# Optimization experiments

Measured on AMD Instinct MI355X. Metric: run time of the kernel, lower is better.

Reference implementation:

```python
import jax, jax.numpy as jnp
import numpy as np

N_NODES = 50000
N_EDGES = 1_600_000
IN_FEAT = 128
OUT_FEAT = 128
NUM_RELS = 8


def setup_inputs() -> dict:
    key = jax.random.key(0)
    k_h, k_src, k_dst, k_et, k_nrm, k_w, k_b = jax.random.split(key, 7)
    h = jax.random.normal(k_h, (N_NODES, IN_FEAT), dtype=jnp.float32)
    src = jax.random.randint(k_src, (N_EDGES,), 0, N_NODES, dtype=jnp.int32)
    dst = jax.random.randint(k_dst, (N_EDGES,), 0, N_NODES, dtype=jnp.int32)
    etype = jax.random.randint(k_et, (N_EDGES,), 0, NUM_RELS, dtype=jnp.int32)
    norm = jax.random.uniform(k_nrm, (N_EDGES, 1), dtype=jnp.float32)
    W = jax.random.normal(k_w, (NUM_RELS, IN_FEAT, OUT_FEAT), dtype=jnp.float32)
    b = jax.random.normal(k_b, (NUM_RELS, OUT_FEAT), dtype=jnp.float32)
    return {"h": h, "src": src, "dst": dst, "etype": etype, "norm": norm, "W": W, "b": b}


def reference(h, src, dst, etype, norm, W, b):
    # Per-relation node transforms: [R, N, out]. Same math as the DGL code
    # (which computes src_h @ W for all relations then gathers the right one
    # per edge), but computed once per node instead of once per edge.
    H = jnp.einsum('ni,rio->rno', h, W)
    # Gather per-edge transformed message, add per-relation bias, scale by norm.
    msg = (H[etype, src] + b[etype]) * norm  # [E, out]
    # Sum-reduce messages into destination nodes.
    out = jax.ops.segment_sum(msg, dst, num_segments=h.shape[0])  # [N, out]
    return jax.nn.relu(out)
```

## Files before the change

### kernel.cpp

```cpp
#include <hip/hip_runtime.h>

#define N_NODES_C   50000
#define N_EDGES_C   1600000
#define FEAT        128
#define NREL        8
#define NBUCKETS    400000
#define KTOT        1024
#define TILE        16

#define WS3_COUNTS   0
#define WS3_OFFSETS  400000
#define WS3_RANK     2000000
#define WS3_BSUM     3600000
#define WS3_BOFF     3602048
#define WS3_SORTED   3604096
#define WS3_HB       10004096
#define WS3_WT       22804096
#define WS3_NEEDED   23066240

typedef __attribute__((ext_vector_type(8))) short bf16x8;
typedef __attribute__((ext_vector_type(4))) float f32x4;

__device__ __forceinline__ unsigned short f2bf(float f) {
    unsigned u = __float_as_uint(f);
    return (unsigned short)((u + 0x7fffu + ((u >> 16) & 1u)) >> 16);
}
__device__ __forceinline__ float bf2f(unsigned short b) {
    return __uint_as_float((unsigned)b << 16);
}
__device__ __forceinline__ float lo16(unsigned u) { return __uint_as_float(u << 16); }
__device__ __forceinline__ float hi16(unsigned u) { return __uint_as_float(u & 0xffff0000u); }

__global__ void k_prep(const float* __restrict__ h, const float* __restrict__ W,
                       unsigned* __restrict__ counts, unsigned short* __restrict__ hb,
                       unsigned short* __restrict__ wt) {
    int b = blockIdx.x, t = threadIdx.x;
    if (b < 3125) {
        int i = (b * 256 + t) * 8;
        float4 v0 = *(const float4*)&h[i];
        float4 v1 = *(const float4*)&h[i + 4];
        uint4 o;
        o.x = (unsigned)f2bf(v0.x) | ((unsigned)f2bf(v0.y) << 16);
        o.y = (unsigned)f2bf(v0.z) | ((unsigned)f2bf(v0.w) << 16);
        o.z = (unsigned)f2bf(v1.x) | ((unsigned)f2bf(v1.y) << 16);
        o.w = (unsigned)f2bf(v1.z) | ((unsigned)f2bf(v1.w) << 16);
        *(uint4*)&hb[i] = o;
    } else if (b < 3125 + 98) {
        int i = (b - 3125) * 256 + t;
        if (i < 25000) ((uint4*)counts)[i] = make_uint4(0u, 0u, 0u, 0u);
    } else {
        int i = (b - 3223) * 256 + t;
        int n = i >> 10, rk = i & 1023;
        wt[i] = f2bf(W[rk * FEAT + n]);
    }
}

__global__ void k_hist(const int* __restrict__ dst, const int* __restrict__ et,
                       unsigned* __restrict__ counts, unsigned char* __restrict__ rank) {
    int e = blockIdx.x * 256 + threadIdx.x;
    if (e < N_EDGES_C) {
        int key = dst[e] * NREL + et[e];
        int sh = 8 * (key & 3);
        unsigned old = atomicAdd(&counts[key >> 2], 1u << sh);
        rank[e] = (unsigned char)((old >> sh) & 0xffu);
    }
}

__global__ void k_scan_a(const unsigned* __restrict__ counts, unsigned* __restrict__ bsum) {
    __shared__ unsigned s[1024];
    int t = threadIdx.x;
    int i = blockIdx.x * 1024 + t;
    unsigned v = 0;
    if (i < NBUCKETS) v = (counts[i >> 2] >> (8 * (i & 3))) & 0xffu;
    s[t] = v;
    __syncthreads();
    for (int o = 512; o > 0; o >>= 1) {
        if (t < o) s[t] += s[t + o];
        __syncthreads();
    }
    if (t == 0) bsum[blockIdx.x] = s[0];
}

__global__ void k_scan_b(const unsigned* __restrict__ bsum, unsigned* __restrict__ boff, int nb) {
    __shared__ unsigned s[512];
    int t = threadIdx.x;
    unsigned v = (t < nb) ? bsum[t] : 0u;
    s[t] = v;
    __syncthreads();
    for (int o = 1; o < 512; o <<= 1) {
        unsigned u = (t >= o) ? s[t - o] : 0u;
        __syncthreads();
        s[t] += u;
        __syncthreads();
    }
    if (t < nb) boff[t] = s[t] - v;
}

__global__ void k_scan_c(const unsigned* __restrict__ counts, const unsigned* __restrict__ boff,
                         unsigned* __restrict__ offsets) {
    __shared__ unsigned s[1024];
    int t = threadIdx.x;
    int i = blockIdx.x * 1024 + t;
    unsigned v = 0;
    if (i < NBUCKETS) v = (counts[i >> 2] >> (8 * (i & 3))) & 0xffu;
    s[t] = v;
    __syncthreads();
    for (int o = 1; o < 1024; o <<= 1) {
        unsigned u = (t >= o) ? s[t - o] : 0u;
        __syncthreads();
        s[t] += u;
        __syncthreads();
    }
    if (i < NBUCKETS) offsets[i] = boff[blockIdx.x] + s[t] - v;
}

__global__ void k_scatter(const int* __restrict__ src, const int* __restrict__ dst,
                          const int* __restrict__ et, const float* __restrict__ norm,
                          const unsigned* __restrict__ offsets,
                          const unsigned char* __restrict__ rank,
                          unsigned* __restrict__ sorted) {
    int e = blockIdx.x * 256 + threadIdx.x;
    if (e < N_EDGES_C) {
        int key = dst[e] * NREL + et[e];
        unsigned pos = offsets[key] + (unsigned)rank[e];
        sorted[pos] = ((unsigned)src[e] << 16) | (unsigned)f2bf(norm[e]);
    }
}

__global__ __launch_bounds__(256) void k_fused(const unsigned* __restrict__ sorted,
                                               const unsigned* __restrict__ offsets,
                                               const unsigned* __restrict__ counts,
                                               const unsigned short* __restrict__ hb,
                                               const unsigned short* __restrict__ wt,
                                               const float* __restrict__ bias,
                                               float* __restrict__ out) {
    __shared__ char At[4096];
    __shared__ float csLds[TILE][NREL];
    int t = threadIdx.x, w = t >> 6, lane = t & 63;
    int node0 = blockIdx.x * TILE;
    int grp  = lane >> 4;
    int ln16 = lane & 15;

    f32x4 acc[2];
    acc[0] = (f32x4){0.f, 0.f, 0.f, 0.f};
    acc[1] = (f32x4){0.f, 0.f, 0.f, 0.f};

#pragma unroll 1
    for (int r = 0; r < NREL; r++) {
#pragma unroll 1
        for (int nn = 0; nn < 4; nn++) {
            int n = w * 4 + nn;
            int key = (node0 + n) * NREL + r;
            unsigned st  = offsets[key];
            unsigned cnt = (counts[key >> 2] >> (8 * (key & 3))) & 0xffu;
            unsigned en  = st + cnt;
            float a0 = 0.f, a1 = 0.f, cs = 0.f;
            unsigned i = st;
            while (i + 2 <= en) {
                unsigned r0 = sorted[i], r1 = sorted[i + 1];
                float n0 = bf2f((unsigned short)(r0 & 0xffffu));
                float n1 = bf2f((unsigned short)(r1 & 0xffffu));
                unsigned hv0 = *(const unsigned*)&hb[(size_t)(r0 >> 16) * FEAT + lane * 2];
                unsigned hv1 = *(const unsigned*)&hb[(size_t)(r1 >> 16) * FEAT + lane * 2];
                a0 += n0 * lo16(hv0) + n1 * lo16(hv1);
                a1 += n0 * hi16(hv0) + n1 * hi16(hv1);
                cs += n0 + n1;
                i += 2;
            }
            if (i < en) {
                unsigned r0 = sorted[i];
                float n0 = bf2f((unsigned short)(r0 & 0xffffu));
                unsigned hv0 = *(const unsigned*)&hb[(size_t)(r0 >> 16) * FEAT + lane * 2];
                a0 += n0 * lo16(hv0);
                a1 += n0 * hi16(hv0);
                cs += n0;
            }
            *(unsigned*)(At + ((n * 256 + lane * 4) ^ ((n & 7) << 4))) =
                (unsigned)f2bf(a0) | ((unsigned)f2bf(a1) << 16);
            if (lane == 0) csLds[n][r] = cs;
        }
        __syncthreads();

        const unsigned short* wr = wt + r * FEAT;
#pragma unroll
        for (int ks = 0; ks < 4; ks++) {
            bf16x8 af = *(const bf16x8*)(At + ((ln16 * 256 + ks * 64 + grp * 16) ^ ((ln16 & 7) << 4)));
#pragma unroll
            for (int c = 0; c < 2; c++) {
                int ncol = (w * 2 + c) * 16 + ln16;
                bf16x8 bf = *(const bf16x8*)(wr + (size_t)ncol * KTOT + ks * 32 + grp * 8);
                acc[c] = __builtin_amdgcn_mfma_f32_16x16x32_bf16(af, bf, acc[c], 0, 0, 0);
            }
        }
        __syncthreads();
    }

#pragma unroll
    for (int i = 0; i < 4; i++) {
        int rl = grp * 4 + i;
        int g  = node0 + rl;
        float cs[NREL];
#pragma unroll
        for (int rr = 0; rr < NREL; rr++) cs[rr] = csLds[rl][rr];
#pragma unroll
        for (int c = 0; c < 2; c++) {
            int col = (w * 2 + c) * 16 + ln16;
            float v = acc[c][i];
#pragma unroll
            for (int rr = 0; rr < NREL; rr++) v += cs[rr] * bias[rr * FEAT + col];
            out[(size_t)g * FEAT + col] = fmaxf(v, 0.f);
        }
    }
}

extern "C" void kernel_launch(void* const* d_in, const int* in_sizes, int n_in,
                              void* d_out, int out_size, void* d_ws, size_t ws_size,
                              hipStream_t stream) {
    const float* h    = (const float*)d_in[0];
    const int*   src  = (const int*)d_in[1];
    const int*   dst  = (const int*)d_in[2];
    const int*   et   = (const int*)d_in[3];
    const float* norm = (const float*)d_in[4];
    const float* W    = (const float*)d_in[5];
    const float* b    = (const float*)d_in[6];
    float*       out  = (float*)d_out;

    if (ws_size < (size_t)WS3_NEEDED) return;

    char* ws = (char*)d_ws;
    unsigned*       counts  = (unsigned*)(ws + WS3_COUNTS);
    unsigned*       offsets = (unsigned*)(ws + WS3_OFFSETS);
    unsigned char*  rank    = (unsigned char*)(ws + WS3_RANK);
    unsigned*       bsum    = (unsigned*)(ws + WS3_BSUM);
    unsigned*       boff    = (unsigned*)(ws + WS3_BOFF);
    unsigned*       sorted  = (unsigned*)(ws + WS3_SORTED);
    unsigned short* hb      = (unsigned short*)(ws + WS3_HB);
    unsigned short* wt      = (unsigned short*)(ws + WS3_WT);

    int nb = (NBUCKETS + 1023) / 1024;

    k_prep<<<3125 + 98 + 512, 256, 0, stream>>>(h, W, counts, hb, wt);
    k_hist<<<6250, 256, 0, stream>>>(dst, et, counts, rank);
    k_scan_a<<<nb, 1024, 0, stream>>>(counts, bsum);
    k_scan_b<<<1, 512, 0, stream>>>(bsum, boff, nb);
    k_scan_c<<<nb, 1024, 0, stream>>>(counts, boff, offsets);
    k_scatter<<<6250, 256, 0, stream>>>(src, dst, et, norm, offsets, rank, sorted);

    k_fused<<<N_NODES_C / TILE, 256, 0, stream>>>(sorted, offsets, counts,
                                                  hb, wt, b, out);
}
```

Baseline: 321.4 us.

## Interleave four node gather streams, single K=1024 MFMA pass, XCD-partitioned scatter

The fused kernel now processes each node's eight relation segments as one contiguous edge run. Each wave interleaves four nodes' streams, prefetching the next sorted record, so there are more independent gathers in flight and fewer barriers. All eight relations' aggregates are staged in a 32KB LDS tile and multiplied in one 32-step MFMA loop instead of eight separate phases. The scatter kernel is split so each XCD group writes only its own key range, aiming for L2 locality on the sorted array, at the cost of every block reading its edges eight times. A sentinel offset is added at NBUCKETS so segment ends come from offsets alone, and the counts argument is dropped.

```diff
diff --git a/kernel.cpp b/kernel.cpp
--- a/kernel.cpp
+++ b/kernel.cpp
@@ -8,15 +8,15 @@
 #define KTOT        1024
 #define TILE        16
 
-#define WS3_COUNTS   0
-#define WS3_OFFSETS  400000
-#define WS3_RANK     2000000
-#define WS3_BSUM     3600000
-#define WS3_BOFF     3602048
-#define WS3_SORTED   3604096
-#define WS3_HB       10004096
-#define WS3_WT       22804096
-#define WS3_NEEDED   23066240
+#define WS_COUNTS   0
+#define WS_OFFSETS  400000
+#define WS_RANK     2000016
+#define WS_BSUM     3600016
+#define WS_BOFF     3602064
+#define WS_SORTED   3604112
+#define WS_HB       10004112
+#define WS_WT       22804112
+#define WS_NEEDED   23066256
 
 typedef __attribute__((ext_vector_type(8))) short bf16x8;
 typedef __attribute__((ext_vector_type(4))) float f32x4;
@@ -112,6 +112,7 @@
         __syncthreads();
     }
     if (i < NBUCKETS) offsets[i] = boff[blockIdx.x] + s[t] - v;
+    if (i == NBUCKETS) offsets[i] = N_EDGES_C;
 }
 
 __global__ void k_scatter(const int* __restrict__ src, const int* __restrict__ dst,
@@ -119,95 +120,119 @@
                           const unsigned* __restrict__ offsets,
                           const unsigned char* __restrict__ rank,
                           unsigned* __restrict__ sorted) {
-    int e = blockIdx.x * 256 + threadIdx.x;
-    if (e < N_EDGES_C) {
+    int xcd = blockIdx.x & 7;
+    int blk = blockIdx.x >> 3;
+    int keyLo = xcd * (NBUCKETS / 8);
+    int keyHi = keyLo + (NBUCKETS / 8);
+    int e0 = blk * 2048;
+    int e1 = e0 + 2048; if (e1 > N_EDGES_C) e1 = N_EDGES_C;
+    for (int e = e0 + threadIdx.x; e < e1; e += 256) {
         int key = dst[e] * NREL + et[e];
-        unsigned pos = offsets[key] + (unsigned)rank[e];
-        sorted[pos] = ((unsigned)src[e] << 16) | (unsigned)f2bf(norm[e]);
+        if (key >= keyLo && key < keyHi) {
+            unsigned pos = offsets[key] + (unsigned)rank[e];
+            sorted[pos] = ((unsigned)src[e] << 16) | (unsigned)f2bf(norm[e]);
+        }
     }
 }
 
 __global__ __launch_bounds__(256) void k_fused(const unsigned* __restrict__ sorted,
                                                const unsigned* __restrict__ offsets,
-                                               const unsigned* __restrict__ counts,
                                                const unsigned short* __restrict__ hb,
                                                const unsigned short* __restrict__ wt,
                                                const float* __restrict__ bias,
                                                float* __restrict__ out) {
-    __shared__ char At[4096];
+    __shared__ char At[32768];
     __shared__ float csLds[TILE][NREL];
     int t = threadIdx.x, w = t >> 6, lane = t & 63;
     int node0 = blockIdx.x * TILE;
-    int grp  = lane >> 4;
-    int ln16 = lane & 15;
+    int grp = lane >> 4, ln16 = lane & 15;
+
+    int kbase = (node0 + w * 4) * NREL;
+    unsigned myofs = offsets[kbase + (lane < 33 ? lane : 32)];
+
+    float a0[4], a1[4], cs[4];
+    unsigned p[4], bend[4], rec[4];
+    int j[4];
+    bool live[4];
+
+#pragma unroll
+    for (int s = 0; s < 4; s++) {
+        int row = w * 4 + s;
+        a0[s] = a1[s] = cs[s] = 0.f;
+        p[s] = __shfl(myofs, s * 8);
+        j[s] = 0;
+        while (j[s] < 8) {
+            bend[s] = __shfl(myofs, s * 8 + j[s] + 1);
+            if (p[s] < bend[s]) break;
+            *(unsigned*)(At + ((row * 2048 + j[s] * 256 + lane * 4) ^ ((row & 7) << 4))) = 0u;
+            if (lane == 0) csLds[row][j[s]] = 0.f;
+            j[s]++;
+        }
+        live[s] = (j[s] < 8);
+        rec[s] = live[s] ? sorted[p[s]] : 0u;
+    }
+
+    while (live[0] | live[1] | live[2] | live[3]) {
+#pragma unroll
+        for (int s = 0; s < 4; s++) {
+            if (!live[s]) continue;
+            int row = w * 4 + s;
+            unsigned rc = rec[s];
+            p[s]++;
+            unsigned pn = (p[s] < N_EDGES_C) ? p[s] : (N_EDGES_C - 1);
+            unsigned recn = sorted[pn];
+            float nv = bf2f((unsigned short)(rc & 0xffffu));
+            unsigned hv = *(const unsigned*)&hb[(size_t)(rc >> 16) * FEAT + lane * 2];
+            a0[s] += nv * lo16(hv);
+            a1[s] += nv * hi16(hv);
+            cs[s] += nv;
+            rec[s] = recn;
+            if (p[s] >= bend[s]) {
+                *(unsigned*)(At + ((row * 2048 + j[s] * 256 + lane * 4) ^ ((row & 7) << 4))) =
+                    (unsigned)f2bf(a0[s]) | ((unsigned)f2bf(a1[s]) << 16);
+                if (lane == 0) csLds[row][j[s]] = cs[s];
+                a0[s] = a1[s] = cs[s] = 0.f;
+                j[s]++;
+                while (j[s] < 8) {
+                    bend[s] = __shfl(myofs, s * 8 + j[s] + 1);
+                    if (p[s] < bend[s]) break;
+                    *(unsigned*)(At + ((row * 2048 + j[s] * 256 + lane * 4) ^ ((row & 7) << 4))) = 0u;
+                    if (lane == 0) csLds[row][j[s]] = 0.f;
+                    j[s]++;
+                }
+                live[s] = (j[s] < 8);
+            }
+        }
+    }
+    __syncthreads();
 
     f32x4 acc[2];
     acc[0] = (f32x4){0.f, 0.f, 0.f, 0.f};
     acc[1] = (f32x4){0.f, 0.f, 0.f, 0.f};
-
-#pragma unroll 1
-    for (int r = 0; r < NREL; r++) {
-#pragma unroll 1
-        for (int nn = 0; nn < 4; nn++) {
-            int n = w * 4 + nn;
-            int key = (node0 + n) * NREL + r;
-            unsigned st  = offsets[key];
-            unsigned cnt = (counts[key >> 2] >> (8 * (key & 3))) & 0xffu;
-            unsigned en  = st + cnt;
-            float a0 = 0.f, a1 = 0.f, cs = 0.f;
-            unsigned i = st;
-            while (i + 2 <= en) {
-                unsigned r0 = sorted[i], r1 = sorted[i + 1];
-                float n0 = bf2f((unsigned short)(r0 & 0xffffu));
-                float n1 = bf2f((unsigned short)(r1 & 0xffffu));
-                unsigned hv0 = *(const unsigned*)&hb[(size_t)(r0 >> 16) * FEAT + lane * 2];
-                unsigned hv1 = *(const unsigned*)&hb[(size_t)(r1 >> 16) * FEAT + lane * 2];
-                a0 += n0 * lo16(hv0) + n1 * lo16(hv1);
-                a1 += n0 * hi16(hv0) + n1 * hi16(hv1);
-                cs += n0 + n1;
-                i += 2;
-            }
-            if (i < en) {
-                unsigned r0 = sorted[i];
-                float n0 = bf2f((unsigned short)(r0 & 0xffffu));
-                unsigned hv0 = *(const unsigned*)&hb[(size_t)(r0 >> 16) * FEAT + lane * 2];
-                a0 += n0 * lo16(hv0);
-                a1 += n0 * hi16(hv0);
-                cs += n0;
-            }
-            *(unsigned*)(At + ((n * 256 + lane * 4) ^ ((n & 7) << 4))) =
-                (unsigned)f2bf(a0) | ((unsigned)f2bf(a1) << 16);
-            if (lane == 0) csLds[n][r] = cs;
-        }
-        __syncthreads();
-
-        const unsigned short* wr = wt + r * FEAT;
-#pragma unroll
-        for (int ks = 0; ks < 4; ks++) {
-            bf16x8 af = *(const bf16x8*)(At + ((ln16 * 256 + ks * 64 + grp * 16) ^ ((ln16 & 7) << 4)));
-#pragma unroll
-            for (int c = 0; c < 2; c++) {
-                int ncol = (w * 2 + c) * 16 + ln16;
-                bf16x8 bf = *(const bf16x8*)(wr + (size_t)ncol * KTOT + ks * 32 + grp * 8);
-                acc[c] = __builtin_amdgcn_mfma_f32_16x16x32_bf16(af, bf, acc[c], 0, 0, 0);
-            }
-        }
-        __syncthreads();
+#pragma unroll 8
+    for (int ks = 0; ks < 32; ks++) {
+        bf16x8 af = *(const bf16x8*)(At + ((ln16 * 2048 + ks * 64 + grp * 16) ^ ((ln16 & 7) << 4)));
+#pragma unroll
+        for (int c = 0; c < 2; c++) {
+            int ncol = (w * 2 + c) * 16 + ln16;
+            bf16x8 bf = *(const bf16x8*)(wt + (size_t)ncol * KTOT + ks * 32 + grp * 8);
+            acc[c] = __builtin_amdgcn_mfma_f32_16x16x32_bf16(af, bf, acc[c], 0, 0, 0);
+        }
     }
 
 #pragma unroll
     for (int i = 0; i < 4; i++) {
         int rl = grp * 4 + i;
         int g  = node0 + rl;
-        float cs[NREL];
-#pragma unroll
-        for (int rr = 0; rr < NREL; rr++) cs[rr] = csLds[rl][rr];
+        float csv[NREL];
+#pragma unroll
+        for (int rr = 0; rr < NREL; rr++) csv[rr] = csLds[rl][rr];
 #pragma unroll
         for (int c = 0; c < 2; c++) {
             int col = (w * 2 + c) * 16 + ln16;
             float v = acc[c][i];
 #pragma unroll
-            for (int rr = 0; rr < NREL; rr++) v += cs[rr] * bias[rr * FEAT + col];
+            for (int rr = 0; rr < NREL; rr++) v += csv[rr] * bias[rr * FEAT + col];
             out[(size_t)g * FEAT + col] = fmaxf(v, 0.f);
         }
     }
@@ -225,17 +250,17 @@
     const float* b    = (const float*)d_in[6];
     float*       out  = (float*)d_out;
 
-    if (ws_size < (size_t)WS3_NEEDED) return;
+    if (ws_size < (size_t)WS_NEEDED) return;
 
     char* ws = (char*)d_ws;
-    unsigned*       counts  = (unsigned*)(ws + WS3_COUNTS);
-    unsigned*       offsets = (unsigned*)(ws + WS3_OFFSETS);
-    unsigned char*  rank    = (unsigned char*)(ws + WS3_RANK);
-    unsigned*       bsum    = (unsigned*)(ws + WS3_BSUM);
-    unsigned*       boff    = (unsigned*)(ws + WS3_BOFF);
-    unsigned*       sorted  = (unsigned*)(ws + WS3_SORTED);
-    unsigned short* hb      = (unsigned short*)(ws + WS3_HB);
-    unsigned short* wt      = (unsigned short*)(ws + WS3_WT);
+    unsigned*       counts  = (unsigned*)(ws + WS_COUNTS);
+    unsigned*       offsets = (unsigned*)(ws + WS_OFFSETS);
+    unsigned char*  rank    = (unsigned char*)(ws + WS_RANK);
+    unsigned*       bsum    = (unsigned*)(ws + WS_BSUM);
+    unsigned*       boff    = (unsigned*)(ws + WS_BOFF);
+    unsigned*       sorted  = (unsigned*)(ws + WS_SORTED);
+    unsigned short* hb      = (unsigned short*)(ws + WS_HB);
+    unsigned short* wt      = (unsigned short*)(ws + WS_WT);
 
     int nb = (NBUCKETS + 1023) / 1024;
 
@@ -244,8 +269,7 @@
     k_scan_a<<<nb, 1024, 0, stream>>>(counts, bsum);
     k_scan_b<<<1, 512, 0, stream>>>(bsum, boff, nb);
     k_scan_c<<<nb, 1024, 0, stream>>>(counts, boff, offsets);
-    k_scatter<<<6250, 256, 0, stream>>>(src, dst, et, norm, offsets, rank, sorted);
-
-    k_fused<<<N_NODES_C / TILE, 256, 0, stream>>>(sorted, offsets, counts,
-                                                  hb, wt, b, out);
-}
+    k_scatter<<<8 * 782, 256, 0, stream>>>(src, dst, et, norm, offsets, rank, sorted);
+
+    k_fused<<<N_NODES_C / TILE, 256, 0, stream>>>(sorted, offsets, hb, wt, b, out);
+}
```

After: 437.1 us. 1.36x slower.
